# Optimization experiments

Measured on AMD Instinct MI355X. Metric: run time of the kernel, lower is better.

## Reference

```python
import jax, jax.numpy as jnp
import numpy as np

VOCAB = 128
HIDDEN = 1024

def setup_inputs() -> dict:
    key = jax.random.key(0)
    kx, ku, kw, kl, kb = jax.random.split(key, 5)
    B, S = 64, 512
    X = jax.random.randint(kx, (B, S), 0, VOCAB)
    # xavier_uniform bounds
    bu = float(np.sqrt(6.0 / (HIDDEN + HIDDEN)))
    bw = float(np.sqrt(6.0 / (HIDDEN + VOCAB)))
    U = jax.random.uniform(ku, (HIDDEN, HIDDEN), minval=-bu, maxval=bu, dtype=jnp.float32)
    W = jax.random.uniform(kw, (HIDDEN, VOCAB), minval=-bw, maxval=bw, dtype=jnp.float32)
    # nn.Linear(hidden, vocab): weight [vocab, hidden], bias [vocab]
    bl = float(1.0 / np.sqrt(HIDDEN))
    lin_w = jax.random.uniform(kl, (VOCAB, HIDDEN), minval=-bl, maxval=bl, dtype=jnp.float32)
    lin_b = jax.random.uniform(kb, (VOCAB,), minval=-bl, maxval=bl, dtype=jnp.float32)
    return {"X": X, "U": U, "W": W, "lin_w": lin_w, "lin_b": lin_b}

def reference(X, U, W, lin_w, lin_b):
    B, S = X.shape
    # one-hot embedding (use_embedding=False path)
    X_emb = jax.nn.one_hot(X, VOCAB, dtype=jnp.float32)  # [B,S,V]
    # precompute input contribution for all steps: x_t @ W.T -> [B,S,H]
    inp = jnp.einsum('bsv,hv->bsh', X_emb, W)
    h0 = jnp.zeros((B, HIDDEN), dtype=jnp.float32)

    def step(h, inp_t):
        h_new = jnp.tanh(h @ U.T + inp_t)  # [B,H]
        return h_new, h_new

    _, hs = jax.lax.scan(step, h0, jnp.swapaxes(inp, 0, 1))  # hs: [S,B,H]
    hs = jnp.swapaxes(hs, 0, 1)  # [B,S,H]
    logits = jnp.einsum('bsh,vh->bsv', hs, lin_w) + lin_b  # [B,S,V]
    return jax.nn.softmax(logits, axis=-1)
```

## Files before the change

kernel.cpp:

```cpp
#include <hip/hip_runtime.h>
#include <cstdint>

static constexpr int Hdim = 1024;
static constexpr int Vdim = 128;
static constexpr int Bdim = 64;
static constexpr int Sdim = 512;

static constexpr int NB   = 8;
static constexpr int NI   = 16;
static constexpr int KCH  = 32;
static constexpr int SL   = 1028;
static constexpr int NBLK = 512;
static constexpr int BPC  = 64;
static constexpr int NCL  = 8;

__global__ void __launch_bounds__(256) pack_u_kernel(const float* __restrict__ U,
                                                     float* __restrict__ Up) {
  __shared__ float tile[16][257];
  const int s  = blockIdx.x;
  const int k0 = blockIdx.y * 256;
  const int t  = threadIdx.x;
  #pragma unroll
  for (int r = 0; r < 16; ++r)
    tile[r][t] = U[(size_t)(s * 16 + r) * Hdim + k0 + t];
  __syncthreads();
  const size_t base = ((size_t)s * Hdim + k0) * 16;
  #pragma unroll
  for (int r2 = 0; r2 < 16; ++r2) {
    int g = r2 * 256 + t;
    Up[base + g] = tile[g & 15][g >> 4];
  }
}

__global__ void transpose_w_kernel(const float* __restrict__ in, float* __restrict__ out) {
  __shared__ float tile[32][33];
  const int bx = blockIdx.x * 32;
  const int by = blockIdx.y * 32;
  const int tx = threadIdx.x, ty = threadIdx.y;
  #pragma unroll
  for (int dy = 0; dy < 32; dy += 8)
    tile[ty + dy][tx] = in[(size_t)(by + ty + dy) * Vdim + bx + tx];
  __syncthreads();
  #pragma unroll
  for (int dy = 0; dy < 32; dy += 8)
    out[(size_t)(bx + ty + dy) * Hdim + by + tx] = tile[tx][ty + dy];
}

__global__ void __launch_bounds__(256, 2) rnn_persist_kernel(
    const float* __restrict__ Up,
    const float* __restrict__ Wt,
    const int*   __restrict__ X,
    const float* __restrict__ lw,
    const float* __restrict__ lb,
    float* __restrict__ h0,
    float* __restrict__ h1,
    unsigned int* __restrict__ flags,
    float* __restrict__ out)
{
  __shared__ float hsm[NB * SL];
  __shared__ float part[4][NB][NI];
  __shared__ float partv[4][NB][2];

  const int tid  = threadIdx.x;
  const int blk  = blockIdx.x;
  const int cl   = blk >> 6;
  const int s    = ((blk & 7) << 3) | ((blk >> 3) & 7);
  const int i0   = s * NI;
  const int bg0  = cl * NB;
  const int kp   = tid >> 3;
  const int b    = tid & 7;
  const int w    = tid >> 6;
  const int lane = tid & 63;
  const float* Ublk = Up + (size_t)s * Hdim * NI;

  auto stage_h = [&](int t) {
    if (t == 0) {
      #pragma unroll
      for (int r = 0; r < NB; ++r) {
        float* dst = &hsm[r * SL + tid * 4];
        dst[0] = 0.f; dst[1] = 0.f; dst[2] = 0.f; dst[3] = 0.f;
      }
    } else {
      const float* hc = (t & 1) ? h1 : h0;
      const unsigned long long* src8 =
          (const unsigned long long*)(hc + (size_t)bg0 * Hdim);
      #pragma unroll
      for (int r = 0; r < NB; ++r) {
        unsigned long long u0 = __hip_atomic_load(&src8[r * (Hdim / 2) + tid * 2],
                                                  __ATOMIC_RELAXED, __HIP_MEMORY_SCOPE_SYSTEM);
        unsigned long long u1 = __hip_atomic_load(&src8[r * (Hdim / 2) + tid * 2 + 1],
                                                  __ATOMIC_RELAXED, __HIP_MEMORY_SCOPE_SYSTEM);
        unsigned long long* dst = (unsigned long long*)&hsm[r * SL + tid * 4];
        dst[0] = u0; dst[1] = u1;
      }
    }
  };

  auto logits_partial = [&]() {
    float a0 = 0.f, a1 = 0.f;
    const float4* lw0 = (const float4*)(lw + (size_t)(2 * s)     * Hdim + kp * KCH);
    const float4* lw1 = (const float4*)(lw + (size_t)(2 * s + 1) * Hdim + kp * KCH);
    const float* hr = &hsm[b * SL + kp * KCH];
    #pragma unroll
    for (int j = 0; j < KCH / 4; ++j) {
      int jj = (j + kp) & (KCH / 4 - 1);
      float4 hv = *((const float4*)&hr[4 * jj]);
      float4 w0 = lw0[jj];
      float4 w1 = lw1[jj];
      a0 += hv.x * w0.x + hv.y * w0.y + hv.z * w0.z + hv.w * w0.w;
      a1 += hv.x * w1.x + hv.y * w1.y + hv.z * w1.z + hv.w * w1.w;
    }
    a0 += __shfl_xor(a0, 8, 64);  a1 += __shfl_xor(a1, 8, 64);
    a0 += __shfl_xor(a0, 16, 64); a1 += __shfl_xor(a1, 16, 64);
    a0 += __shfl_xor(a0, 32, 64); a1 += __shfl_xor(a1, 32, 64);
    if ((lane & 56) == 0) { partv[w][b][0] = a0; partv[w][b][1] = a1; }
  };

  auto logits_combine = [&](int tt) {
    if (tid >= 128 && tid < 128 + 2 * NB) {
      const int q = tid - 128;
      const int bb = q >> 1, vv = q & 1;
      float lv = partv[0][bb][vv] + partv[1][bb][vv] + partv[2][bb][vv] + partv[3][bb][vv];
      lv += lb[2 * s + vv];
      out[((size_t)(bg0 + bb) * Sdim + tt) * Vdim + 2 * s + vv] = lv;
    }
  };

  for (int t = 0; t < Sdim; ++t) {
    stage_h(t);
    __syncthreads();

    {
      float acc[NI];
      #pragma unroll
      for (int i = 0; i < NI; ++i) acc[i] = 0.f;
      const float* hr = &hsm[b * SL + kp * KCH];
      const float4* ub = (const float4*)(Ublk + (size_t)kp * KCH * NI);
      #pragma unroll 4
      for (int j = 0; j < KCH; ++j) {
        int jj = (j + kp) & (KCH - 1);
        float hv = hr[jj];
        const float4* u = ub + (size_t)jj * 4;
        float4 u0 = u[0], u1 = u[1], u2 = u[2], u3 = u[3];
        acc[0]  += u0.x * hv; acc[1]  += u0.y * hv; acc[2]  += u0.z * hv; acc[3]  += u0.w * hv;
        acc[4]  += u1.x * hv; acc[5]  += u1.y * hv; acc[6]  += u1.z * hv; acc[7]  += u1.w * hv;
        acc[8]  += u2.x * hv; acc[9]  += u2.y * hv; acc[10] += u2.z * hv; acc[11] += u2.w * hv;
        acc[12] += u3.x * hv; acc[13] += u3.y * hv; acc[14] += u3.z * hv; acc[15] += u3.w * hv;
      }
      #pragma unroll
      for (int i = 0; i < NI; ++i) {
        acc[i] += __shfl_xor(acc[i], 8, 64);
        acc[i] += __shfl_xor(acc[i], 16, 64);
        acc[i] += __shfl_xor(acc[i], 32, 64);
      }
      if ((lane & 56) == 0) {
        #pragma unroll
        for (int i = 0; i < NI; i += 4)
          *((float4*)&part[w][b][i]) = make_float4(acc[i], acc[i + 1], acc[i + 2], acc[i + 3]);
      }
    }
    __syncthreads();

    if (tid < NB * NI) {
      const int b2 = tid >> 4, i2 = tid & 15;
      float v = part[0][b2][i2] + part[1][b2][i2] + part[2][b2][i2] + part[3][b2][i2];
      const int x = X[(bg0 + b2) * Sdim + t];
      v += Wt[(size_t)x * Hdim + i0 + i2];
      v = tanhf(v);
      float* hn = (t & 1) ? h0 : h1;
      __hip_atomic_store(&hn[(size_t)(bg0 + b2) * Hdim + i0 + i2], v,
                         __ATOMIC_RELAXED, __HIP_MEMORY_SCOPE_SYSTEM);
    }

    asm volatile("s_waitcnt vmcnt(0)" ::: "memory");
    __syncthreads();
    if (tid == 0)
      __hip_atomic_store(&flags[cl * BPC + s], (unsigned)(t + 1),
                         __ATOMIC_RELAXED, __HIP_MEMORY_SCOPE_SYSTEM);

    if (t > 0) logits_partial();
    __syncthreads();
    if (t > 0) logits_combine(t - 1);

    if (tid < 64) {
      const unsigned int tag = (unsigned)(t + 1);
      unsigned int* f = &flags[cl * BPC + tid];
      while (true) {
        unsigned int fv = __hip_atomic_load(f, __ATOMIC_RELAXED, __HIP_MEMORY_SCOPE_SYSTEM);
        if (__all((int)(fv >= tag))) break;
        __builtin_amdgcn_s_sleep(1);
      }
    }
    __syncthreads();
  }

  stage_h(Sdim);
  __syncthreads();
  logits_partial();
  __syncthreads();
  logits_combine(Sdim - 1);
}

__global__ void __launch_bounds__(256) softmax_kernel(float* __restrict__ out) {
  const int row = blockIdx.x * 4 + (threadIdx.x >> 6);
  const int l = threadIdx.x & 63;
  float* rp = out + (size_t)row * Vdim;
  float2 v = *((const float2*)&rp[l * 2]);
  float m = fmaxf(v.x, v.y);
  #pragma unroll
  for (int d = 1; d < 64; d <<= 1) m = fmaxf(m, __shfl_xor(m, d, 64));
  float e0 = expf(v.x - m), e1 = expf(v.y - m);
  float ss = e0 + e1;
  #pragma unroll
  for (int d = 1; d < 64; d <<= 1) ss += __shfl_xor(ss, d, 64);
  const float inv = 1.f / ss;
  *((float2*)&rp[l * 2]) = make_float2(e0 * inv, e1 * inv);
}

extern "C" void kernel_launch(void* const* d_in, const int* in_sizes, int n_in,
                              void* d_out, int out_size, void* d_ws, size_t ws_size,
                              hipStream_t stream) {
  const int*   X  = (const int*)d_in[0];
  const float* U  = (const float*)d_in[1];
  const float* W  = (const float*)d_in[2];
  const float* lw = (const float*)d_in[3];
  const float* lb = (const float*)d_in[4];
  float* out = (float*)d_out;

  float* Up = (float*)d_ws;
  float* Wt = Up + (size_t)1024 * 1024;
  float* h0 = Wt + (size_t)128 * 1024;
  float* h1 = h0 + (size_t)64 * 1024;
  unsigned int* flags = (unsigned int*)(h1 + (size_t)64 * 1024);
  const size_t need = ((size_t)1024 * 1024 + 128 * 1024 + 2 * 64 * 1024) * 4 + NCL * Sdim * 4;
  if (ws_size < need) return;

  hipMemsetAsync(flags, 0, (size_t)NCL * Sdim * sizeof(unsigned int), stream);

  hipLaunchKernelGGL(pack_u_kernel, dim3(64, 4), dim3(256), 0, stream, U, Up);
  hipLaunchKernelGGL(transpose_w_kernel, dim3(4, 32), dim3(32, 8), 0, stream, W, Wt);

  void* args[] = {(void*)&Up, (void*)&Wt, (void*)&X, (void*)&lw, (void*)&lb,
                  (void*)&h0, (void*)&h1, (void*)&flags, (void*)&out};
  hipError_t ce = hipLaunchCooperativeKernel((void*)rnn_persist_kernel,
                                             dim3(NBLK), dim3(256), args, 0, stream);
  if (ce != hipSuccess) {
    hipLaunchKernelGGL(rnn_persist_kernel, dim3(NBLK), dim3(256), 0, stream,
                       Up, Wt, X, lw, lb, h0, h1, flags, out);
  }

  hipLaunchKernelGGL(softmax_kernel, dim3((Bdim * Sdim) / 4), dim3(256), 0, stream, out);
}
```

Before: 6.248 ms.

## Halve persistent RNN block count with wider hidden slices and inline-asm h loads

Each persistent block now owns 32 hidden units instead of 16, so only 256 blocks (32 per batch cluster) run, which shrinks the per-step flag barrier fan-in and the number of blocks to synchronise. The logits projection correspondingly covers 4 vocab entries per block. The h staging loads are replaced with inline-asm global_load_dwordx4 carrying cache-bypass bits in place of 64-bit atomic loads. In exchange each block does twice the U streaming and math per step, register pressure rises with 32 accumulators, and there is half as much total parallelism across CUs.

```diff
diff --git a/kernel.cpp b/kernel.cpp
--- a/kernel.cpp
+++ b/kernel.cpp
@@ -1,5 +1,7 @@
 #include <hip/hip_runtime.h>
 #include <cstdint>
+
+typedef float f32x4 __attribute__((ext_vector_type(4)));
 
 static constexpr int Hdim = 1024;
 static constexpr int Vdim = 128;
@@ -7,28 +9,28 @@
 static constexpr int Sdim = 512;
 
 static constexpr int NB   = 8;
-static constexpr int NI   = 16;
+static constexpr int NI   = 32;
 static constexpr int KCH  = 32;
 static constexpr int SL   = 1028;
-static constexpr int NBLK = 512;
-static constexpr int BPC  = 64;
+static constexpr int NBLK = 256;
+static constexpr int BPC  = 32;
 static constexpr int NCL  = 8;
 
 __global__ void __launch_bounds__(256) pack_u_kernel(const float* __restrict__ U,
                                                      float* __restrict__ Up) {
-  __shared__ float tile[16][257];
+  __shared__ float tile[32][257];
   const int s  = blockIdx.x;
   const int k0 = blockIdx.y * 256;
   const int t  = threadIdx.x;
   #pragma unroll
-  for (int r = 0; r < 16; ++r)
-    tile[r][t] = U[(size_t)(s * 16 + r) * Hdim + k0 + t];
-  __syncthreads();
-  const size_t base = ((size_t)s * Hdim + k0) * 16;
-  #pragma unroll
-  for (int r2 = 0; r2 < 16; ++r2) {
+  for (int r = 0; r < 32; ++r)
+    tile[r][t] = U[(size_t)(s * 32 + r) * Hdim + k0 + t];
+  __syncthreads();
+  const size_t base = ((size_t)s * Hdim + k0) * 32;
+  #pragma unroll
+  for (int r2 = 0; r2 < 32; ++r2) {
     int g = r2 * 256 + t;
-    Up[base + g] = tile[g & 15][g >> 4];
+    Up[base + g] = tile[g & 31][g >> 5];
   }
 }
 
@@ -46,7 +48,7 @@
     out[(size_t)(bx + ty + dy) * Hdim + by + tx] = tile[tx][ty + dy];
 }
 
-__global__ void __launch_bounds__(256, 2) rnn_persist_kernel(
+__global__ void __launch_bounds__(256, 1) rnn_persist_kernel(
     const float* __restrict__ Up,
     const float* __restrict__ Wt,
     const int*   __restrict__ X,
@@ -59,12 +61,12 @@
 {
   __shared__ float hsm[NB * SL];
   __shared__ float part[4][NB][NI];
-  __shared__ float partv[4][NB][2];
+  __shared__ float partv[4][NB][4];
 
   const int tid  = threadIdx.x;
   const int blk  = blockIdx.x;
-  const int cl   = blk >> 6;
-  const int s    = ((blk & 7) << 3) | ((blk >> 3) & 7);
+  const int cl   = blk >> 5;
+  const int s    = blk & 31;
   const int i0   = s * NI;
   const int bg0  = cl * NB;
   const int kp   = tid >> 3;
@@ -75,54 +77,74 @@
 
   auto stage_h = [&](int t) {
     if (t == 0) {
-      #pragma unroll
-      for (int r = 0; r < NB; ++r) {
-        float* dst = &hsm[r * SL + tid * 4];
-        dst[0] = 0.f; dst[1] = 0.f; dst[2] = 0.f; dst[3] = 0.f;
-      }
+      const f32x4 z = (f32x4){0.f, 0.f, 0.f, 0.f};
+      #pragma unroll
+      for (int r = 0; r < NB; ++r)
+        *((f32x4*)&hsm[r * SL + tid * 4]) = z;
     } else {
       const float* hc = (t & 1) ? h1 : h0;
-      const unsigned long long* src8 =
-          (const unsigned long long*)(hc + (size_t)bg0 * Hdim);
-      #pragma unroll
-      for (int r = 0; r < NB; ++r) {
-        unsigned long long u0 = __hip_atomic_load(&src8[r * (Hdim / 2) + tid * 2],
-                                                  __ATOMIC_RELAXED, __HIP_MEMORY_SCOPE_SYSTEM);
-        unsigned long long u1 = __hip_atomic_load(&src8[r * (Hdim / 2) + tid * 2 + 1],
-                                                  __ATOMIC_RELAXED, __HIP_MEMORY_SCOPE_SYSTEM);
-        unsigned long long* dst = (unsigned long long*)&hsm[r * SL + tid * 4];
-        dst[0] = u0; dst[1] = u1;
-      }
+      const float* p = hc + (size_t)bg0 * Hdim + tid * 4;
+      f32x4 v0, v1, v2, v3, v4, v5, v6, v7;
+      asm volatile(
+          "global_load_dwordx4 %0, %8, off sc0 sc1\n\t"
+          "global_load_dwordx4 %1, %9, off sc0 sc1\n\t"
+          "global_load_dwordx4 %2, %10, off sc0 sc1\n\t"
+          "global_load_dwordx4 %3, %11, off sc0 sc1\n\t"
+          "global_load_dwordx4 %4, %12, off sc0 sc1\n\t"
+          "global_load_dwordx4 %5, %13, off sc0 sc1\n\t"
+          "global_load_dwordx4 %6, %14, off sc0 sc1\n\t"
+          "global_load_dwordx4 %7, %15, off sc0 sc1\n\t"
+          "s_waitcnt vmcnt(0)"
+          : "=&v"(v0), "=&v"(v1), "=&v"(v2), "=&v"(v3),
+            "=&v"(v4), "=&v"(v5), "=&v"(v6), "=&v"(v7)
+          : "v"(p), "v"(p + Hdim), "v"(p + 2 * Hdim), "v"(p + 3 * Hdim),
+            "v"(p + 4 * Hdim), "v"(p + 5 * Hdim), "v"(p + 6 * Hdim), "v"(p + 7 * Hdim)
+          : "memory");
+      *((f32x4*)&hsm[0 * SL + tid * 4]) = v0;
+      *((f32x4*)&hsm[1 * SL + tid * 4]) = v1;
+      *((f32x4*)&hsm[2 * SL + tid * 4]) = v2;
+      *((f32x4*)&hsm[3 * SL + tid * 4]) = v3;
+      *((f32x4*)&hsm[4 * SL + tid * 4]) = v4;
+      *((f32x4*)&hsm[5 * SL + tid * 4]) = v5;
+      *((f32x4*)&hsm[6 * SL + tid * 4]) = v6;
+      *((f32x4*)&hsm[7 * SL + tid * 4]) = v7;
     }
   };
 
   auto logits_partial = [&]() {
-    float a0 = 0.f, a1 = 0.f;
-    const float4* lw0 = (const float4*)(lw + (size_t)(2 * s)     * Hdim + kp * KCH);
-    const float4* lw1 = (const float4*)(lw + (size_t)(2 * s + 1) * Hdim + kp * KCH);
-    const float* hr = &hsm[b * SL + kp * KCH];
+    float a0 = 0.f, a1 = 0.f, a2 = 0.f, a3 = 0.f;
+    const f32x4* lw0 = (const f32x4*)(lw + (size_t)(4 * s)     * Hdim + kp * KCH);
+    const f32x4* lw1 = (const f32x4*)(lw + (size_t)(4 * s + 1) * Hdim + kp * KCH);
+    const f32x4* lw2 = (const f32x4*)(lw + (size_t)(4 * s + 2) * Hdim + kp * KCH);
+    const f32x4* lw3 = (const f32x4*)(lw + (size_t)(4 * s + 3) * Hdim + kp * KCH);
+    const f32x4* hr4 = (const f32x4*)&hsm[b * SL + kp * KCH];
     #pragma unroll
     for (int j = 0; j < KCH / 4; ++j) {
       int jj = (j + kp) & (KCH / 4 - 1);
-      float4 hv = *((const float4*)&hr[4 * jj]);
-      float4 w0 = lw0[jj];
-      float4 w1 = lw1[jj];
-      a0 += hv.x * w0.x + hv.y * w0.y + hv.z * w0.z + hv.w * w0.w;
-      a1 += hv.x * w1.x + hv.y * w1.y + hv.z * w1.z + hv.w * w1.w;
-    }
-    a0 += __shfl_xor(a0, 8, 64);  a1 += __shfl_xor(a1, 8, 64);
-    a0 += __shfl_xor(a0, 16, 64); a1 += __shfl_xor(a1, 16, 64);
-    a0 += __shfl_xor(a0, 32, 64); a1 += __shfl_xor(a1, 32, 64);
-    if ((lane & 56) == 0) { partv[w][b][0] = a0; partv[w][b][1] = a1; }
+      f32x4 hv = hr4[jj];
+      f32x4 q0 = lw0[jj], q1 = lw1[jj], q2 = lw2[jj], q3 = lw3[jj];
+      #pragma unroll
+      for (int e = 0; e < 4; ++e) {
+        a0 += hv[e] * q0[e]; a1 += hv[e] * q1[e];
+        a2 += hv[e] * q2[e]; a3 += hv[e] * q3[e];
+      }
+    }
+    #pragma unroll
+    for (int d = 8; d < 64; d <<= 1) {
+      a0 += __shfl_xor(a0, d, 64); a1 += __shfl_xor(a1, d, 64);
+      a2 += __shfl_xor(a2, d, 64); a3 += __shfl_xor(a3, d, 64);
+    }
+    if ((lane & 56) == 0)
+      *((f32x4*)&partv[w][b][0]) = (f32x4){a0, a1, a2, a3};
   };
 
   auto logits_combine = [&](int tt) {
-    if (tid >= 128 && tid < 128 + 2 * NB) {
+    if (tid >= 128 && tid < 128 + 4 * NB) {
       const int q = tid - 128;
-      const int bb = q >> 1, vv = q & 1;
+      const int bb = q >> 2, vv = q & 3;
       float lv = partv[0][bb][vv] + partv[1][bb][vv] + partv[2][bb][vv] + partv[3][bb][vv];
-      lv += lb[2 * s + vv];
-      out[((size_t)(bg0 + bb) * Sdim + tt) * Vdim + 2 * s + vv] = lv;
+      lv += lb[4 * s + vv];
+      out[((size_t)(bg0 + bb) * Sdim + tt) * Vdim + 4 * s + vv] = lv;
     }
   };
 
@@ -135,17 +157,20 @@
       #pragma unroll
       for (int i = 0; i < NI; ++i) acc[i] = 0.f;
       const float* hr = &hsm[b * SL + kp * KCH];
-      const float4* ub = (const float4*)(Ublk + (size_t)kp * KCH * NI);
+      const f32x4* ub = (const f32x4*)(Ublk + (size_t)kp * KCH * NI);
       #pragma unroll 4
       for (int j = 0; j < KCH; ++j) {
         int jj = (j + kp) & (KCH - 1);
         float hv = hr[jj];
-        const float4* u = ub + (size_t)jj * 4;
-        float4 u0 = u[0], u1 = u[1], u2 = u[2], u3 = u[3];
-        acc[0]  += u0.x * hv; acc[1]  += u0.y * hv; acc[2]  += u0.z * hv; acc[3]  += u0.w * hv;
-        acc[4]  += u1.x * hv; acc[5]  += u1.y * hv; acc[6]  += u1.z * hv; acc[7]  += u1.w * hv;
-        acc[8]  += u2.x * hv; acc[9]  += u2.y * hv; acc[10] += u2.z * hv; acc[11] += u2.w * hv;
-        acc[12] += u3.x * hv; acc[13] += u3.y * hv; acc[14] += u3.z * hv; acc[15] += u3.w * hv;
+        const f32x4* u = ub + (size_t)jj * (NI / 4);
+        #pragma unroll
+        for (int q = 0; q < NI / 4; ++q) {
+          const f32x4 uq = u[q];
+          acc[q * 4 + 0] += uq[0] * hv;
+          acc[q * 4 + 1] += uq[1] * hv;
+          acc[q * 4 + 2] += uq[2] * hv;
+          acc[q * 4 + 3] += uq[3] * hv;
+        }
       }
       #pragma unroll
       for (int i = 0; i < NI; ++i) {
@@ -156,13 +181,13 @@
       if ((lane & 56) == 0) {
         #pragma unroll
         for (int i = 0; i < NI; i += 4)
-          *((float4*)&part[w][b][i]) = make_float4(acc[i], acc[i + 1], acc[i + 2], acc[i + 3]);
-      }
-    }
-    __syncthreads();
-
-    if (tid < NB * NI) {
-      const int b2 = tid >> 4, i2 = tid & 15;
+          *((f32x4*)&part[w][b][i]) = (f32x4){acc[i], acc[i + 1], acc[i + 2], acc[i + 3]};
+      }
+    }
+    __syncthreads();
+
+    {
+      const int b2 = tid >> 5, i2 = tid & 31;
       float v = part[0][b2][i2] + part[1][b2][i2] + part[2][b2][i2] + part[3][b2][i2];
       const int x = X[(bg0 + b2) * Sdim + t];
       v += Wt[(size_t)x * Hdim + i0 + i2];
@@ -184,7 +209,7 @@
 
     if (tid < 64) {
       const unsigned int tag = (unsigned)(t + 1);
-      unsigned int* f = &flags[cl * BPC + tid];
+      unsigned int* f = &flags[cl * BPC + (tid & (BPC - 1))];
       while (true) {
         unsigned int fv = __hip_atomic_load(f, __ATOMIC_RELAXED, __HIP_MEMORY_SCOPE_SYSTEM);
         if (__all((int)(fv >= tag))) break;
@@ -232,12 +257,12 @@
   float* h0 = Wt + (size_t)128 * 1024;
   float* h1 = h0 + (size_t)64 * 1024;
   unsigned int* flags = (unsigned int*)(h1 + (size_t)64 * 1024);
-  const size_t need = ((size_t)1024 * 1024 + 128 * 1024 + 2 * 64 * 1024) * 4 + NCL * Sdim * 4;
+  const size_t need = ((size_t)1024 * 1024 + 128 * 1024 + 2 * 64 * 1024) * 4 + NCL * BPC * 4;
   if (ws_size < need) return;
 
-  hipMemsetAsync(flags, 0, (size_t)NCL * Sdim * sizeof(unsigned int), stream);
-
-  hipLaunchKernelGGL(pack_u_kernel, dim3(64, 4), dim3(256), 0, stream, U, Up);
+  hipMemsetAsync(flags, 0, (size_t)NCL * BPC * sizeof(unsigned int), stream);
+
+  hipLaunchKernelGGL(pack_u_kernel, dim3(32, 4), dim3(256), 0, stream, U, Up);
   hipLaunchKernelGGL(transpose_w_kernel, dim3(4, 32), dim3(32, 8), 0, stream, W, Wt);
 
   void* args[] = {(void*)&Up, (void*)&Wt, (void*)&X, (void*)&lw, (void*)&lb,
```

Measured after the change: 6.360 ms. No clear change (+1.8%).
